# Kernel tuning notes

Measured on AMD Instinct MI355X. Metric: run time of the kernel, lower is better.

The kernel has to match this reference:

```python
import jax, jax.numpy as jnp
import numpy as np

PATCH_NUM = 196  # 14*14 patch grid
BASE_NUM = 128

def setup_inputs() -> dict:
    key = jax.random.key(0)
    k1, k2, k3, k4 = jax.random.split(key, 4)
    b = 128
    return {
        "h_scores": jax.random.normal(k1, (b, BASE_NUM, 3, 14), dtype=jnp.float32),
        "v_score": jax.random.normal(k2, (b, BASE_NUM, 3, 14), dtype=jnp.float32),
        "h_base": jax.random.normal(k3, (b, BASE_NUM, 16), dtype=jnp.float32),
        "v_base": jax.random.normal(k4, (b, BASE_NUM, 16), dtype=jnp.float32),
    }

def reference(h_scores, v_score, h_base, v_base):
    b = h_scores.shape[0]
    # base images per base vector: [b, k, m, n]
    base_matrix = jnp.einsum('bkn,bkm->bkmn', h_base, v_base)
    # per-patch, per-channel scores: [b, k, 3, n', m'] -> [b, k, 3, P]
    score = jnp.einsum('bkcn,bkcm->bkcnm', h_scores, v_score)
    score = score.reshape(b, BASE_NUM, 3, PATCH_NUM)
    # [b, P, 3, k]; softmax over base dim (matches per-patch F.softmax(dim=2))
    score = jnp.transpose(score, (0, 3, 2, 1))
    score = jax.nn.softmax(score, axis=-1)
    # weighted sum of base images: [b, P, 3, m, n]
    res = jnp.einsum('bpck,bkmn->bpcmn', score, base_matrix)
    return res
```

## Files before the change

### kernel.cpp

```cpp
#include <hip/hip_runtime.h>

typedef __attribute__((ext_vector_type(8))) short bf16x8;
typedef __attribute__((ext_vector_type(4))) float f32x4;

#define PATCHES 196
#define ROWS 588
#define NCHUNK 10
#define SCORE_B_STRIDE 5376

static __device__ __forceinline__ unsigned f2bf2(float a, float b) {
    union { float f; unsigned u; } x, y; x.f = a; y.f = b;
    unsigned lo = (x.u + 0x7FFFu + ((x.u >> 16) & 1u)) >> 16;
    unsigned hi = (y.u + 0x7FFFu + ((y.u >> 16) & 1u)) & 0xFFFF0000u;
    return lo | hi;
}

__global__ __launch_bounds__(256) void bm_build(
    const float* __restrict__ h_base,
    const float* __restrict__ v_base,
    uint4* __restrict__ bmv)
{
    __shared__ float hbT[16][68];
    __shared__ float vbT[16][68];
    const int b = blockIdx.x, zb = blockIdx.y, t = threadIdx.x;
    const float* hg = h_base + (size_t)b * 2048 + zb * 1024;
    const float* vg = v_base + (size_t)b * 2048 + zb * 1024;
#pragma unroll
    for (int i = 0; i < 4; ++i) {
        const int idx = t + i * 256;
        hbT[idx & 15][idx >> 4] = hg[idx];
        vbT[idx & 15][idx >> 4] = vg[idx];
    }
    __syncthreads();

    const int m = t >> 4, n = t & 15;
    uint4* dst = bmv + ((size_t)b * 16 + zb * 8) * 256 + t;
#pragma unroll
    for (int i = 0; i < 8; ++i) {
        const float* vp = &vbT[m][i * 8];
        const float* hp = &hbT[n][i * 8];
        float p[8];
#pragma unroll
        for (int j = 0; j < 8; ++j) p[j] = vp[j] * hp[j];
        uint4 u = { f2bf2(p[0],p[1]), f2bf2(p[2],p[3]),
                    f2bf2(p[4],p[5]), f2bf2(p[6],p[7]) };
        dst[i * 256] = u;
    }
}

__global__ __launch_bounds__(256, 3) void patch_gemm(
    const float* __restrict__ h_scores,
    const float* __restrict__ v_score,
    const uint4* __restrict__ bmv,
    float* __restrict__ out)
{
    __shared__ __align__(16) char lds[16384];

    const int bid = blockIdx.x;
    const int xcd = bid & 7, rest = bid >> 3;
    const int b = (rest / NCHUNK) * 8 + xcd;
    const int chunk = rest % NCHUNK;
    const int t = threadIdx.x;

    {
        const int r = t >> 2, kq = t & 3;
        const int grow = chunk * 64 + r;
        const int geff = grow < ROWS ? grow : ROWS - 1;
        const int p = geff / 3, c = geff - p * 3;
        const int np = p / 14, mp = p - np * 14;
        const float* hsb = h_scores + (size_t)b * SCORE_B_STRIDE;
        const float* vsb = v_score  + (size_t)b * SCORE_B_STRIDE;
        const int hix = c * 14 + np, vix = c * 14 + mp;

        float sc[32];
#pragma unroll
        for (int j = 0; j < 32; ++j) {
            const int k = kq * 32 + j;
            sc[j] = hsb[k * 42 + hix] * vsb[k * 42 + vix];
        }
        float mx = sc[0];
#pragma unroll
        for (int j = 1; j < 32; ++j) mx = fmaxf(mx, sc[j]);
        mx = fmaxf(mx, __shfl_xor(mx, 1));
        mx = fmaxf(mx, __shfl_xor(mx, 2));
        float sum = 0.f;
#pragma unroll
        for (int j = 0; j < 32; ++j) { sc[j] = __expf(sc[j] - mx); sum += sc[j]; }
        sum += __shfl_xor(sum, 1);
        sum += __shfl_xor(sum, 2);
        const float inv = 1.f / sum;

        const int sw = (r & 7) << 4;
#pragma unroll
        for (int s2 = 0; s2 < 4; ++s2) {
            const int kpos = (kq * 32 + s2 * 8) * 2;
            uint4 u = { f2bf2(sc[s2*8+0]*inv, sc[s2*8+1]*inv),
                        f2bf2(sc[s2*8+2]*inv, sc[s2*8+3]*inv),
                        f2bf2(sc[s2*8+4]*inv, sc[s2*8+5]*inv),
                        f2bf2(sc[s2*8+6]*inv, sc[s2*8+7]*inv) };
            *(uint4*)(lds + r * 256 + (kpos ^ sw)) = u;
        }
    }
    __syncthreads();

    const int w = t >> 6, lane = t & 63;
    const int wrh = w >> 1, wnh = w & 1;
    const int lr = lane & 15, lg = lane >> 4;

    bf16x8 wfrag[2][4];
#pragma unroll
    for (int mi = 0; mi < 2; ++mi) {
        const int r2 = wrh * 32 + mi * 16 + lr;
        const int sw = (r2 & 7) << 4;
#pragma unroll
        for (int kc = 0; kc < 4; ++kc)
            wfrag[mi][kc] = *(const bf16x8*)(lds + r2 * 256 + ((kc * 64 + lg * 16) ^ sw));
    }

    const uint4* bmb = bmv + (size_t)b * 4096;

    f32x4 acc[2][8];
#pragma unroll
    for (int mi = 0; mi < 2; ++mi)
#pragma unroll
        for (int nt = 0; nt < 8; ++nt)
            acc[mi][nt] = (f32x4){0.f, 0.f, 0.f, 0.f};

#pragma unroll
    for (int nt = 0; nt < 8; ++nt) {
        const int mn = wnh * 128 + nt * 16 + lr;
#pragma unroll
        for (int kc = 0; kc < 4; ++kc) {
            uint4 raw = bmb[(kc * 4 + lg) * 256 + mn];
            bf16x8 bfrag = *(bf16x8*)&raw;
            acc[0][nt] = __builtin_amdgcn_mfma_f32_16x16x32_bf16(bfrag, wfrag[0][kc], acc[0][nt], 0, 0, 0);
            acc[1][nt] = __builtin_amdgcn_mfma_f32_16x16x32_bf16(bfrag, wfrag[1][kc], acc[1][nt], 0, 0, 0);
        }
    }

    float* ob = out + (size_t)b * (ROWS * 256);
#pragma unroll
    for (int mi = 0; mi < 2; ++mi) {
        const int gr = chunk * 64 + wrh * 32 + mi * 16 + lr;
        if (gr < ROWS) {
            float* orow = ob + (size_t)gr * 256 + wnh * 128 + lg * 4;
#pragma unroll
            for (int nt = 0; nt < 8; ++nt)
                __builtin_nontemporal_store(acc[mi][nt], (f32x4*)(orow + nt * 16));
        }
    }
}

extern "C" void kernel_launch(void* const* d_in, const int* in_sizes, int n_in,
                              void* d_out, int out_size, void* d_ws, size_t ws_size,
                              hipStream_t stream) {
    const float* h_scores = (const float*)d_in[0];
    const float* v_score  = (const float*)d_in[1];
    const float* h_base   = (const float*)d_in[2];
    const float* v_base   = (const float*)d_in[3];
    float* out = (float*)d_out;
    uint4* bmv = (uint4*)d_ws;

    const int B = in_sizes[0] / SCORE_B_STRIDE;

    bm_build<<<dim3(B, 2), 256, 0, stream>>>(h_base, v_base, bmv);
    patch_gemm<<<B * NCHUNK, 256, 0, stream>>>(h_scores, v_score, bmv, out);
}
```

Measured before the change: 35.53 us.

## Fuse base-matrix build into patch GEMM kernel with LDS-staged scores

Merges the two kernels into one. Each 512-thread block now builds its half of the bf16 base matrix directly in LDS instead of reading it from a workspace, and stages the score rows in LDS so they are read with vector loads. Tiles change to 128 rows by 128 columns, and batches are mapped contiguously per XCD. This removes a kernel launch and the workspace round trip, at the cost of each block recomputing base-matrix slices and a larger LDS footprint (64KB), which lowers occupancy.

Result: no change. 35.82 us (+0.8%).

```diff
diff --git a/kernel.cpp b/kernel.cpp
--- a/kernel.cpp
+++ b/kernel.cpp
@@ -3,10 +3,10 @@
 typedef __attribute__((ext_vector_type(8))) short bf16x8;
 typedef __attribute__((ext_vector_type(4))) float f32x4;
 
-#define PATCHES 196
 #define ROWS 588
-#define NCHUNK 10
-#define SCORE_B_STRIDE 5376
+#define SSTRIDE 5376
+#define OUT_B 150528
+
 
 static __device__ __forceinline__ unsigned f2bf2(float a, float b) {
     union { float f; unsigned u; } x, y; x.f = a; y.f = b;
@@ -15,68 +15,77 @@
     return lo | hi;
 }
 
-__global__ __launch_bounds__(256) void bm_build(
+__global__ __launch_bounds__(512, 4) void fused_patch(
+    const float* __restrict__ h_scores,
+    const float* __restrict__ v_score,
     const float* __restrict__ h_base,
     const float* __restrict__ v_base,
-    uint4* __restrict__ bmv)
+    float* __restrict__ out,
+    int bd8)
 {
-    __shared__ float hbT[16][68];
-    __shared__ float vbT[16][68];
-    const int b = blockIdx.x, zb = blockIdx.y, t = threadIdx.x;
-    const float* hg = h_base + (size_t)b * 2048 + zb * 1024;
-    const float* vg = v_base + (size_t)b * 2048 + zb * 1024;
+    __shared__ __align__(16) char lds[65536];
+
+    const int bid = blockIdx.x;
+    const int xcd = bid & 7, idx = bid >> 3;
+    const int b   = xcd * bd8 + idx / 10;
+    const int sub = idx % 10;
+    const int hh  = sub & 1;
+    const int ch  = sub >> 1;
+    const int t = threadIdx.x;
+
+    {
+        const float* vg = v_base + (size_t)b * 2048;
+        const float* hg = h_base + (size_t)b * 2048;
+        const int mn = t & 127, kcq = t >> 7;
+        const int m_g = hh * 8 + (mn >> 4), n = mn & 15;
 #pragma unroll
-    for (int i = 0; i < 4; ++i) {
-        const int idx = t + i * 256;
-        hbT[idx & 15][idx >> 4] = hg[idx];
-        vbT[idx & 15][idx >> 4] = vg[idx];
+        for (int ii = 0; ii < 4; ++ii) {
+            const int kc8 = kcq * 4 + ii;
+            float p[8];
+#pragma unroll
+            for (int j = 0; j < 8; ++j) {
+                const int k = kc8 * 8 + j;
+                p[j] = vg[k * 16 + m_g] * hg[k * 16 + n];
+            }
+            uint4 u = { f2bf2(p[0],p[1]), f2bf2(p[2],p[3]),
+                        f2bf2(p[4],p[5]), f2bf2(p[6],p[7]) };
+            *(uint4*)(lds + (kc8 * 128 + mn) * 16) = u;
+        }
+    }
+
+    const int pmin = (ch * 128) / 3;
+    const int np0  = pmin / 14;
+    {
+        const float* hs_b = h_scores + (size_t)b * SSTRIDE;
+        const float* vs_b = v_score  + (size_t)b * SSTRIDE;
+        float* hT = (float*)(lds + 32768);
+        float* vT = (float*)(lds + 39104);
+        for (int e = t; e < 1536; e += 512) {
+            const int k = e / 12, cc = e - k * 12;
+            hT[cc * 132 + k] = hs_b[k * 42 + (cc >> 2) * 14 + np0 + (cc & 3)];
+        }
+        for (int e = t; e < 5376; e += 512) {
+            const int k = e / 42, col = e - k * 42;
+            vT[col * 132 + k] = vs_b[e];
+        }
     }
     __syncthreads();
 
-    const int m = t >> 4, n = t & 15;
-    uint4* dst = bmv + ((size_t)b * 16 + zb * 8) * 256 + t;
-#pragma unroll
-    for (int i = 0; i < 8; ++i) {
-        const float* vp = &vbT[m][i * 8];
-        const float* hp = &hbT[n][i * 8];
-        float p[8];
-#pragma unroll
-        for (int j = 0; j < 8; ++j) p[j] = vp[j] * hp[j];
-        uint4 u = { f2bf2(p[0],p[1]), f2bf2(p[2],p[3]),
-                    f2bf2(p[4],p[5]), f2bf2(p[6],p[7]) };
-        dst[i * 256] = u;
-    }
-}
-
-__global__ __launch_bounds__(256, 3) void patch_gemm(
-    const float* __restrict__ h_scores,
-    const float* __restrict__ v_score,
-    const uint4* __restrict__ bmv,
-    float* __restrict__ out)
-{
-    __shared__ __align__(16) char lds[16384];
-
-    const int bid = blockIdx.x;
-    const int xcd = bid & 7, rest = bid >> 3;
-    const int b = (rest / NCHUNK) * 8 + xcd;
-    const int chunk = rest % NCHUNK;
-    const int t = threadIdx.x;
-
+    const int r = t >> 2, kq = t & 3;
+    float sc[32];
+    float inv;
     {
-        const int r = t >> 2, kq = t & 3;
-        const int grow = chunk * 64 + r;
+        const int grow = ch * 128 + r;
         const int geff = grow < ROWS ? grow : ROWS - 1;
         const int p = geff / 3, c = geff - p * 3;
         const int np = p / 14, mp = p - np * 14;
-        const float* hsb = h_scores + (size_t)b * SCORE_B_STRIDE;
-        const float* vsb = v_score  + (size_t)b * SCORE_B_STRIDE;
-        const int hix = c * 14 + np, vix = c * 14 + mp;
-
-        float sc[32];
+        const f32x4* hp = (const f32x4*)(lds + 32768 + ((c * 4 + np - np0) * 132 + kq * 32) * 4);
+        const f32x4* vp = (const f32x4*)(lds + 39104 + ((c * 14 + mp) * 132 + kq * 32) * 4);
 #pragma unroll
-        for (int j = 0; j < 32; ++j) {
-            const int k = kq * 32 + j;
-            sc[j] = hsb[k * 42 + hix] * vsb[k * 42 + vix];
+        for (int j4 = 0; j4 < 8; ++j4) {
+            f32x4 h4 = hp[j4], v4 = vp[j4];
+#pragma unroll
+            for (int e = 0; e < 4; ++e) sc[j4 * 4 + e] = h4[e] * v4[e];
         }
         float mx = sc[0];
 #pragma unroll
@@ -88,64 +97,64 @@
         for (int j = 0; j < 32; ++j) { sc[j] = __expf(sc[j] - mx); sum += sc[j]; }
         sum += __shfl_xor(sum, 1);
         sum += __shfl_xor(sum, 2);
-        const float inv = 1.f / sum;
+        inv = 1.f / sum;
+    }
+    __syncthreads();
 
+    {
         const int sw = (r & 7) << 4;
 #pragma unroll
         for (int s2 = 0; s2 < 4; ++s2) {
-            const int kpos = (kq * 32 + s2 * 8) * 2;
+            const int kpos = kq * 64 + s2 * 16;
             uint4 u = { f2bf2(sc[s2*8+0]*inv, sc[s2*8+1]*inv),
                         f2bf2(sc[s2*8+2]*inv, sc[s2*8+3]*inv),
                         f2bf2(sc[s2*8+4]*inv, sc[s2*8+5]*inv),
                         f2bf2(sc[s2*8+6]*inv, sc[s2*8+7]*inv) };
-            *(uint4*)(lds + r * 256 + (kpos ^ sw)) = u;
+            *(uint4*)(lds + 32768 + r * 256 + (kpos ^ sw)) = u;
         }
     }
     __syncthreads();
 
     const int w = t >> 6, lane = t & 63;
-    const int wrh = w >> 1, wnh = w & 1;
+    const int wr = w >> 1, wh = w & 1;
     const int lr = lane & 15, lg = lane >> 4;
 
     bf16x8 wfrag[2][4];
 #pragma unroll
     for (int mi = 0; mi < 2; ++mi) {
-        const int r2 = wrh * 32 + mi * 16 + lr;
+        const int r2 = (wr * 2 + mi) * 16 + lr;
         const int sw = (r2 & 7) << 4;
 #pragma unroll
         for (int kc = 0; kc < 4; ++kc)
-            wfrag[mi][kc] = *(const bf16x8*)(lds + r2 * 256 + ((kc * 64 + lg * 16) ^ sw));
+            wfrag[mi][kc] = *(const bf16x8*)(lds + 32768 + r2 * 256 + ((kc * 64 + lg * 16) ^ sw));
     }
 
-    const uint4* bmb = bmv + (size_t)b * 4096;
-
-    f32x4 acc[2][8];
+    f32x4 acc[2][4];
 #pragma unroll
     for (int mi = 0; mi < 2; ++mi)
 #pragma unroll
-        for (int nt = 0; nt < 8; ++nt)
+        for (int nt = 0; nt < 4; ++nt)
             acc[mi][nt] = (f32x4){0.f, 0.f, 0.f, 0.f};
 
 #pragma unroll
-    for (int nt = 0; nt < 8; ++nt) {
-        const int mn = wnh * 128 + nt * 16 + lr;
+    for (int nt = 0; nt < 4; ++nt) {
+        const int mnl = wh * 64 + nt * 16 + lr;
 #pragma unroll
         for (int kc = 0; kc < 4; ++kc) {
-            uint4 raw = bmb[(kc * 4 + lg) * 256 + mn];
-            bf16x8 bfrag = *(bf16x8*)&raw;
+            bf16x8 bfrag = *(const bf16x8*)(lds + ((kc * 4 + lg) * 128 + mnl) * 16);
             acc[0][nt] = __builtin_amdgcn_mfma_f32_16x16x32_bf16(bfrag, wfrag[0][kc], acc[0][nt], 0, 0, 0);
             acc[1][nt] = __builtin_amdgcn_mfma_f32_16x16x32_bf16(bfrag, wfrag[1][kc], acc[1][nt], 0, 0, 0);
         }
     }
 
-    float* ob = out + (size_t)b * (ROWS * 256);
+    float* ob = out + (size_t)b * OUT_B;
 #pragma unroll
     for (int mi = 0; mi < 2; ++mi) {
-        const int gr = chunk * 64 + wrh * 32 + mi * 16 + lr;
+        const int gr = ch * 128 + (wr * 2 + mi) * 16 + lr;
         if (gr < ROWS) {
-            float* orow = ob + (size_t)gr * 256 + wnh * 128 + lg * 4;
+            float* orow = ob + (size_t)gr * 256 + hh * 128 + wh * 64 + lg * 4;
 #pragma unroll
-            for (int nt = 0; nt < 8; ++nt)
+            for (int nt = 0; nt < 4; ++nt)
                 __builtin_nontemporal_store(acc[mi][nt], (f32x4*)(orow + nt * 16));
         }
     }
@@ -159,10 +168,7 @@
     const float* h_base   = (const float*)d_in[2];
     const float* v_base   = (const float*)d_in[3];
     float* out = (float*)d_out;
-    uint4* bmv = (uint4*)d_ws;
 
-    const int B = in_sizes[0] / SCORE_B_STRIDE;
-
-    bm_build<<<dim3(B, 2), 256, 0, stream>>>(h_base, v_base, bmv);
-    patch_gemm<<<B * NCHUNK, 256, 0, stream>>>(h_scores, v_score, bmv, out);
+    const int B = in_sizes[0] / SSTRIDE;
+    fused_patch<<<B * 10, 512, 0, stream>>>(h_scores, v_score, h_base, v_base, out, B / 8);
 }
```

## Move softmax score computation into prep kernel and DMA weights into LDS

Applied to the files above, without the earlier changes.

The per-patch score product, softmax and bf16 packing move out of the GEMM kernel into the prep kernel. The prep kernel stages whole score rows in shared memory and writes swizzled bf16 weight tiles to workspace. The GEMM kernel then fills LDS directly with global_load_lds, which removes the strided score gathers and softmax from its critical path. In exchange, the prep kernel has far fewer blocks doing heavy serial work, and each weight row makes an extra round trip through global memory.

New measurement: 54.53 us. +53.5%, slower.

```diff
diff --git a/kernel.cpp b/kernel.cpp
--- a/kernel.cpp
+++ b/kernel.cpp
@@ -3,10 +3,11 @@
 typedef __attribute__((ext_vector_type(8))) short bf16x8;
 typedef __attribute__((ext_vector_type(4))) float f32x4;
 
-#define PATCHES 196
 #define ROWS 588
+#define WROWS 640
 #define NCHUNK 10
-#define SCORE_B_STRIDE 5376
+#define SSTRIDE 5376
+#define WB_BYTES 163840
 
 static __device__ __forceinline__ unsigned f2bf2(float a, float b) {
     union { float f; unsigned u; } x, y; x.f = a; y.f = b;
@@ -15,42 +16,96 @@
     return lo | hi;
 }
 
-__global__ __launch_bounds__(256) void bm_build(
+__global__ __launch_bounds__(512) void prep(
+    const float* __restrict__ h_scores,
+    const float* __restrict__ v_score,
     const float* __restrict__ h_base,
     const float* __restrict__ v_base,
-    uint4* __restrict__ bmv)
+    uint4* __restrict__ bmv,
+    char* __restrict__ w_ws)
 {
-    __shared__ float hbT[16][68];
-    __shared__ float vbT[16][68];
+    __shared__ float hbT[16][68], vbT[16][68];
+    __shared__ float sh[SSTRIDE], sv[SSTRIDE];
     const int b = blockIdx.x, zb = blockIdx.y, t = threadIdx.x;
+
     const float* hg = h_base + (size_t)b * 2048 + zb * 1024;
     const float* vg = v_base + (size_t)b * 2048 + zb * 1024;
 #pragma unroll
-    for (int i = 0; i < 4; ++i) {
-        const int idx = t + i * 256;
+    for (int i = 0; i < 2; ++i) {
+        const int idx = t + i * 512;
         hbT[idx & 15][idx >> 4] = hg[idx];
         vbT[idx & 15][idx >> 4] = vg[idx];
     }
+    const float* hsb = h_scores + (size_t)b * SSTRIDE;
+    const float* vsb = v_score  + (size_t)b * SSTRIDE;
+    for (int e = t; e < SSTRIDE; e += 512) { sh[e] = hsb[e]; sv[e] = vsb[e]; }
     __syncthreads();
 
-    const int m = t >> 4, n = t & 15;
-    uint4* dst = bmv + ((size_t)b * 16 + zb * 8) * 256 + t;
+    {
+        const int mn = t & 255, kq2 = t >> 8;
+        const int m = mn >> 4, n = mn & 15;
+        uint4* dst = bmv + ((size_t)b * 16 + zb * 8 + kq2 * 4) * 256 + mn;
 #pragma unroll
-    for (int i = 0; i < 8; ++i) {
-        const float* vp = &vbT[m][i * 8];
-        const float* hp = &hbT[n][i * 8];
-        float p[8];
+        for (int i = 0; i < 4; ++i) {
+            const int kp = (kq2 * 4 + i) * 8;
+            float p[8];
 #pragma unroll
-        for (int j = 0; j < 8; ++j) p[j] = vp[j] * hp[j];
-        uint4 u = { f2bf2(p[0],p[1]), f2bf2(p[2],p[3]),
-                    f2bf2(p[4],p[5]), f2bf2(p[6],p[7]) };
-        dst[i * 256] = u;
+            for (int j = 0; j < 8; ++j) p[j] = vbT[m][kp + j] * hbT[n][kp + j];
+            uint4 u = { f2bf2(p[0],p[1]), f2bf2(p[2],p[3]),
+                        f2bf2(p[4],p[5]), f2bf2(p[6],p[7]) };
+            dst[i * 256] = u;
+        }
+    }
+
+    char* wb = w_ws + (size_t)b * WB_BYTES;
+    const int r2 = t >> 1, kh = t & 1;
+    const int lim = zb ? 346 : 294;
+#pragma unroll
+    for (int rr = 0; rr < 2; ++rr) {
+        const int local = rr * 256 + r2;
+        if (local < lim) {
+            const int grow = zb * 294 + local;
+            const int sw = (grow & 7) << 4;
+            char* wrow = wb + grow * 256;
+            if (grow < ROWS) {
+                const int p = grow / 3, c = grow - p * 3;
+                const int np = p / 14, mp = p - np * 14;
+                const int hix = c * 14 + np, vix = c * 14 + mp;
+                float sc[64];
+#pragma unroll
+                for (int j = 0; j < 64; ++j) {
+                    const int k = kh * 64 + j;
+                    sc[j] = sh[k * 42 + hix] * sv[k * 42 + vix];
+                }
+                float mx = sc[0];
+#pragma unroll
+                for (int j = 1; j < 64; ++j) mx = fmaxf(mx, sc[j]);
+                mx = fmaxf(mx, __shfl_xor(mx, 1));
+                float sum = 0.f;
+#pragma unroll
+                for (int j = 0; j < 64; ++j) { sc[j] = __expf(sc[j] - mx); sum += sc[j]; }
+                sum += __shfl_xor(sum, 1);
+                const float inv = 1.f / sum;
+#pragma unroll
+                for (int s = 0; s < 8; ++s) {
+                    uint4 u = { f2bf2(sc[s*8+0]*inv, sc[s*8+1]*inv),
+                                f2bf2(sc[s*8+2]*inv, sc[s*8+3]*inv),
+                                f2bf2(sc[s*8+4]*inv, sc[s*8+5]*inv),
+                                f2bf2(sc[s*8+6]*inv, sc[s*8+7]*inv) };
+                    *(uint4*)(wrow + ((kh * 128 + s * 16) ^ sw)) = u;
+                }
+            } else {
+                uint4 z = {0u, 0u, 0u, 0u};
+#pragma unroll
+                for (int s = 0; s < 8; ++s)
+                    *(uint4*)(wrow + ((kh * 128 + s * 16) ^ sw)) = z;
+            }
+        }
     }
 }
 
-__global__ __launch_bounds__(256, 3) void patch_gemm(
-    const float* __restrict__ h_scores,
-    const float* __restrict__ v_score,
+__global__ __launch_bounds__(256) void patch_gemm(
+    const char* __restrict__ w_ws,
     const uint4* __restrict__ bmv,
     float* __restrict__ out)
 {
@@ -61,49 +116,20 @@
     const int b = (rest / NCHUNK) * 8 + xcd;
     const int chunk = rest % NCHUNK;
     const int t = threadIdx.x;
+    const int w = t >> 6, lane = t & 63;
 
     {
-        const int r = t >> 2, kq = t & 3;
-        const int grow = chunk * 64 + r;
-        const int geff = grow < ROWS ? grow : ROWS - 1;
-        const int p = geff / 3, c = geff - p * 3;
-        const int np = p / 14, mp = p - np * 14;
-        const float* hsb = h_scores + (size_t)b * SCORE_B_STRIDE;
-        const float* vsb = v_score  + (size_t)b * SCORE_B_STRIDE;
-        const int hix = c * 14 + np, vix = c * 14 + mp;
-
-        float sc[32];
+        const char* src = w_ws + (size_t)b * WB_BYTES + chunk * 16384;
 #pragma unroll
-        for (int j = 0; j < 32; ++j) {
-            const int k = kq * 32 + j;
-            sc[j] = hsb[k * 42 + hix] * vsb[k * 42 + vix];
-        }
-        float mx = sc[0];
-#pragma unroll
-        for (int j = 1; j < 32; ++j) mx = fmaxf(mx, sc[j]);
-        mx = fmaxf(mx, __shfl_xor(mx, 1));
-        mx = fmaxf(mx, __shfl_xor(mx, 2));
-        float sum = 0.f;
-#pragma unroll
-        for (int j = 0; j < 32; ++j) { sc[j] = __expf(sc[j] - mx); sum += sc[j]; }
-        sum += __shfl_xor(sum, 1);
-        sum += __shfl_xor(sum, 2);
-        const float inv = 1.f / sum;
-
-        const int sw = (r & 7) << 4;
-#pragma unroll
-        for (int s2 = 0; s2 < 4; ++s2) {
-            const int kpos = (kq * 32 + s2 * 8) * 2;
-            uint4 u = { f2bf2(sc[s2*8+0]*inv, sc[s2*8+1]*inv),
-                        f2bf2(sc[s2*8+2]*inv, sc[s2*8+3]*inv),
-                        f2bf2(sc[s2*8+4]*inv, sc[s2*8+5]*inv),
-                        f2bf2(sc[s2*8+6]*inv, sc[s2*8+7]*inv) };
-            *(uint4*)(lds + r * 256 + (kpos ^ sw)) = u;
+        for (int i = 0; i < 4; ++i) {
+            const int off = i * 4096 + w * 1024;
+            __builtin_amdgcn_global_load_lds(
+                (const __attribute__((address_space(1))) void*)(src + off + lane * 16),
+                (__attribute__((address_space(3))) void*)(lds + off), 16, 0, 0);
         }
     }
     __syncthreads();
 
-    const int w = t >> 6, lane = t & 63;
     const int wrh = w >> 1, wnh = w & 1;
     const int lr = lane & 15, lg = lane >> 4;
 
@@ -159,10 +185,12 @@
     const float* h_base   = (const float*)d_in[2];
     const float* v_base   = (const float*)d_in[3];
     float* out = (float*)d_out;
+
+    const int B = in_sizes[0] / SSTRIDE;
+
     uint4* bmv = (uint4*)d_ws;
+    char* w_ws = (char*)d_ws + (size_t)8 * 1024 * 1024;
 
-    const int B = in_sizes[0] / SCORE_B_STRIDE;
-
-    bm_build<<<dim3(B, 2), 256, 0, stream>>>(h_base, v_base, bmv);
-    patch_gemm<<<B * NCHUNK, 256, 0, stream>>>(h_scores, v_score, bmv, out);
+    prep<<<dim3(B, 2), 512, 0, stream>>>(h_scores, v_score, h_base, v_base, bmv, w_ws);
+    patch_gemm<<<B * NCHUNK, 256, 0, stream>>>(w_ws, bmv, out);
 }
```
